# Performance work log

Measured on AMD Instinct MI355X. Metric: run time of the kernel, lower is better.

## Reference

```python
import jax, jax.numpy as jnp
import numpy as np

N = 100000   # nodes
E = 1600000  # edges
NF, EF = 128, 16      # node_features, edge_features
NFIL, EFIL = 64, 32   # node_filters, edge_filters
C = 16                # classes


def setup_inputs() -> dict:
    key = jax.random.key(0)
    ks = jax.random.split(key, 12)
    s = 0.1
    return {
        "x": jax.random.normal(ks[0], (N, NF), jnp.float32),
        "edge_index": jax.random.randint(ks[1], (2, E), 0, N),
        "edge_x": jax.random.normal(ks[2], (E, EF), jnp.float32),
        # edge MLP params
        "W1": jax.random.normal(ks[3], (EF, EFIL), jnp.float32) * s,
        "b1": jnp.zeros((EFIL,), jnp.float32),
        "W2": jax.random.normal(ks[4], (EFIL, 1), jnp.float32) * s,
        "b2": jnp.zeros((1,), jnp.float32),
        # GCN layer params
        "Wc1": jax.random.normal(ks[5], (NF, NFIL), jnp.float32) * s,
        "bc1": jnp.zeros((NFIL,), jnp.float32),
        "Wc2": jax.random.normal(ks[6], (NFIL, C), jnp.float32) * s,
        "bc2": jnp.zeros((C,), jnp.float32),
    }


def gcn_conv(x, src, tgt, w, W, b, n):
    # PyG GCNConv with edge_weight: x @ W, symmetric norm, scatter-add, + bias.
    x = x @ W                                             # [n, out]
    deg = jax.ops.segment_sum(w, tgt, num_segments=n)     # weighted degree incl. self-loops
    dinv = jnp.where(deg > 0, jax.lax.rsqrt(deg), 0.0)
    norm = dinv[src] * w * dinv[tgt]                      # [E+n]
    out = jax.ops.segment_sum(norm[:, None] * x[src], tgt, num_segments=n)
    return out + b


def reference(x, edge_index, edge_x, W1, b1, W2, b2, Wc1, bc1, Wc2, bc2):
    # edge MLP -> scalar attention weight per edge
    h = jax.nn.relu(edge_x @ W1 + b1)
    ew = jax.nn.sigmoid(h @ W2 + b2).reshape(-1)          # [E]
    src, tgt = edge_index[0], edge_index[1]
    # add self-loops with weight 1 (as GCNConv does internally)
    loop = jnp.arange(N)
    src_f = jnp.concatenate([src, loop])
    tgt_f = jnp.concatenate([tgt, loop])
    ew_f = jnp.concatenate([ew, jnp.ones((N,), ew.dtype)])
    h1 = jax.nn.relu(gcn_conv(x, src_f, tgt_f, ew_f, Wc1, bc1, N))
    # dropout omitted: eval mode (F.dropout is identity when training=False)
    h2 = gcn_conv(h1, src_f, tgt_f, ew_f, Wc2, bc2, N)
    return jax.nn.log_softmax(h2, axis=1)
```

## Files before the change

### kernel.cpp

```cpp
#include <hip/hip_runtime.h>
#include <math.h>

#define NFD 128
#define EF_ 16
#define EFIL 32
#define NFIL 64
#define CLS 16

typedef unsigned int uint;
typedef unsigned long long ull;
typedef unsigned short ushort;

__device__ inline void fma4(float4& a, float s, const float4& w) {
  a.x = fmaf(s, w.x, a.x); a.y = fmaf(s, w.y, a.y);
  a.z = fmaf(s, w.z, a.z); a.w = fmaf(s, w.w, a.w);
}

__device__ inline uint bf16_rn(float f) {
  uint u = __float_as_uint(f);
  return (u + 0x7FFFu + ((u >> 16) & 1u)) >> 16;
}
__device__ inline float entw(uint lo) {
  return __uint_as_float((lo >> 17) << 16);
}

__global__ void init_head_kernel(int* __restrict__ head, int n) {
  int i = blockIdx.x * blockDim.x + threadIdx.x;
  if (i < n) head[i] = -1;
}

__global__ __launch_bounds__(256) void edge_mlp_link_kernel(
    const float* __restrict__ edge_x, const int* __restrict__ ei,
    const float* __restrict__ W1, const float* __restrict__ b1,
    const float* __restrict__ W2, const float* __restrict__ b2,
    int* __restrict__ head, ull* __restrict__ nextbuf, int E) {
  __shared__ __align__(16) float sW1[EF_ * EFIL];
  __shared__ float sb1[EFIL];
  __shared__ float sW2[EFIL];
  __shared__ float sb2v;
  int t = threadIdx.x;
  for (int idx = t; idx < EF_ * EFIL / 4; idx += 256)
    reinterpret_cast<float4*>(sW1)[idx] = reinterpret_cast<const float4*>(W1)[idx];
  if (t < EFIL) { sb1[t] = b1[t]; sW2[t] = W2[t]; }
  if (t == 64) sb2v = b2[0];
  __syncthreads();
  int e = blockIdx.x * 256 + t;
  if (e >= E) return;
  const float4* ex4 = reinterpret_cast<const float4*>(edge_x) + (size_t)e * (EF_ / 4);
  float ex[EF_];
  #pragma unroll
  for (int q = 0; q < EF_ / 4; q++) {
    float4 v = ex4[q];
    ex[4*q+0] = v.x; ex[4*q+1] = v.y; ex[4*q+2] = v.z; ex[4*q+3] = v.w;
  }
  float acc[EFIL];
  #pragma unroll
  for (int j = 0; j < EFIL; j++) acc[j] = sb1[j];
  #pragma unroll
  for (int k = 0; k < EF_; k++) {
    float xk = ex[k];
    #pragma unroll
    for (int j4 = 0; j4 < EFIL / 4; j4++) {
      float4 w = reinterpret_cast<const float4*>(sW1)[k * (EFIL/4) + j4];
      acc[4*j4+0] = fmaf(xk, w.x, acc[4*j4+0]);
      acc[4*j4+1] = fmaf(xk, w.y, acc[4*j4+1]);
      acc[4*j4+2] = fmaf(xk, w.z, acc[4*j4+2]);
      acc[4*j4+3] = fmaf(xk, w.w, acc[4*j4+3]);
    }
  }
  float s = sb2v;
  #pragma unroll
  for (int j = 0; j < EFIL; j++) s = fmaf(fmaxf(acc[j], 0.f), sW2[j], s);
  float sig = 1.0f / (1.0f + __expf(-s));
  int sv = ei[e], tg = ei[(size_t)E + e];
  uint lo = ((bf16_rn(sig) & 0x7FFFu) << 17) | (uint)sv;
  int old = atomicExch(&head[tg], e);
  nextbuf[e] = ((ull)(uint)old << 32) | lo;
}

__global__ __launch_bounds__(256) void walk_kernel(
    const int* __restrict__ head, const ull* __restrict__ nextbuf,
    uint* __restrict__ slot, int* __restrict__ grp_cnt,
    float* __restrict__ dinv, int cap, int n) {
  int i = blockIdx.x * blockDim.x + threadIdx.x;
  if (i >= n) return;
  int e = head[i];
  int cnt = 0;
  float sum = 0.f;
  uint* sl = slot + (size_t)i * cap;
  while (e >= 0 && cnt < cap) {
    uint b0 = 0, b1 = 0, b2 = 0, b3 = 0, b4 = 0, b5 = 0, b6 = 0, b7 = 0;
    int k = 0;
    ull v;
    v = nextbuf[e]; b0 = (uint)v; sum += entw(b0); e = (int)(uint)(v >> 32); k = 1;
    if (e >= 0) { v = nextbuf[e]; b1 = (uint)v; sum += entw(b1); e = (int)(uint)(v >> 32); k = 2;
    if (e >= 0) { v = nextbuf[e]; b2 = (uint)v; sum += entw(b2); e = (int)(uint)(v >> 32); k = 3;
    if (e >= 0) { v = nextbuf[e]; b3 = (uint)v; sum += entw(b3); e = (int)(uint)(v >> 32); k = 4;
    if (e >= 0) { v = nextbuf[e]; b4 = (uint)v; sum += entw(b4); e = (int)(uint)(v >> 32); k = 5;
    if (e >= 0) { v = nextbuf[e]; b5 = (uint)v; sum += entw(b5); e = (int)(uint)(v >> 32); k = 6;
    if (e >= 0) { v = nextbuf[e]; b6 = (uint)v; sum += entw(b6); e = (int)(uint)(v >> 32); k = 7;
    if (e >= 0) { v = nextbuf[e]; b7 = (uint)v; sum += entw(b7); e = (int)(uint)(v >> 32); k = 8;
    }}}}}}}
    uint4 lov = {b0, b1, b2, b3};
    uint4 hiv = {b4, b5, b6, b7};
    *reinterpret_cast<uint4*>(sl + cnt) = lov;
    *reinterpret_cast<uint4*>(sl + cnt + 4) = hiv;
    cnt += k;
  }
  grp_cnt[i] = cnt;
  dinv[i] = rsqrtf(1.0f + sum);
}

__global__ __launch_bounds__(256) void gemm1_kernel(
    const float* __restrict__ x, const float* __restrict__ Wc1,
    uint* __restrict__ xwb, int n) {
  __shared__ __align__(16) float sW[NFD * NFIL];
  int t = threadIdx.x;
  for (int idx = t; idx < NFD * NFIL / 4; idx += 256)
    reinterpret_cast<float4*>(sW)[idx] = reinterpret_cast<const float4*>(Wc1)[idx];
  __syncthreads();
  int tc = t & 15;
  int tr = t >> 4;
  int nrb = (n + 31) >> 5;
  const float4* sW4 = reinterpret_cast<const float4*>(sW);
  for (int rb = blockIdx.x; rb < nrb; rb += gridDim.x) {
    int r0 = rb * 32 + tr * 2;
    int r1 = r0 + 1;
    int c0 = r0 < n ? r0 : n - 1;
    int c1 = r1 < n ? r1 : n - 1;
    const float4* xr0 = reinterpret_cast<const float4*>(x + (size_t)c0 * NFD);
    const float4* xr1 = reinterpret_cast<const float4*>(x + (size_t)c1 * NFD);
    float4 a0 = {0, 0, 0, 0}, a1 = {0, 0, 0, 0};
    #pragma unroll 4
    for (int k4 = 0; k4 < NFD / 4; k4++) {
      float4 xa = xr0[k4];
      float4 xb = xr1[k4];
      float4 w0 = sW4[(k4*4+0)*16 + tc];
      float4 w1 = sW4[(k4*4+1)*16 + tc];
      float4 w2 = sW4[(k4*4+2)*16 + tc];
      float4 w3 = sW4[(k4*4+3)*16 + tc];
      fma4(a0, xa.x, w0); fma4(a0, xa.y, w1); fma4(a0, xa.z, w2); fma4(a0, xa.w, w3);
      fma4(a1, xb.x, w0); fma4(a1, xb.y, w1); fma4(a1, xb.z, w2); fma4(a1, xb.w, w3);
    }
    if (r0 < n) {
      uint2 o = {bf16_rn(a0.x) | (bf16_rn(a0.y) << 16),
                 bf16_rn(a0.z) | (bf16_rn(a0.w) << 16)};
      reinterpret_cast<uint2*>(xwb + (size_t)r0 * 32)[tc] = o;
    }
    if (r1 < n) {
      uint2 o = {bf16_rn(a1.x) | (bf16_rn(a1.y) << 16),
                 bf16_rn(a1.z) | (bf16_rn(a1.w) << 16)};
      reinterpret_cast<uint2*>(xwb + (size_t)r1 * 32)[tc] = o;
    }
  }
}

__global__ __launch_bounds__(256) void agg1_fused_kernel(
    const int* __restrict__ grp_cnt, const uint* __restrict__ slot, int cap,
    const float* __restrict__ dinv, const uint* __restrict__ xwb,
    const float* __restrict__ bc1, const float* __restrict__ Wc2,
    ushort* __restrict__ ywb, int n) {
  __shared__ float sh[16][NFIL + 4];
  __shared__ float sW2[NFIL * CLS];
  __shared__ float sb1[NFIL];
  int t = threadIdx.x;
  for (int i = t; i < NFIL * CLS; i += 256) sW2[i] = Wc2[i];
  if (t < NFIL) sb1[t] = bc1[t];
  __syncthreads();
  int r = t >> 4;
  int node = blockIdx.x * 16 + r;
  int f4 = t & 15;
  bool ok = node < n;
  int nd = ok ? node : 0;
  int cnt = ok ? grp_cnt[nd] : 0;
  const uint* base = slot + (size_t)nd * cap;
  const uint2* xw2 = reinterpret_cast<const uint2*>(xwb);
  float d = ok ? dinv[nd] : 0.f;
  uint2 g = xw2[(size_t)nd * 16 + f4];
  float4 acc = {d * __uint_as_float(g.x << 16),
                d * __uint_as_float(g.x & 0xFFFF0000u),
                d * __uint_as_float(g.y << 16),
                d * __uint_as_float(g.y & 0xFFFF0000u)};
  int p = 0;
  for (; p + 1 < cnt; p += 2) {
    uint v0 = base[p], v1 = base[p + 1];
    int s0 = v0 & 0x1FFFF, s1 = v1 & 0x1FFFF;
    float w0 = entw(v0) * dinv[s0];
    float w1 = entw(v1) * dinv[s1];
    uint2 g0 = xw2[(size_t)s0 * 16 + f4];
    uint2 g1 = xw2[(size_t)s1 * 16 + f4];
    acc.x = fmaf(w0, __uint_as_float(g0.x << 16), acc.x);
    acc.y = fmaf(w0, __uint_as_float(g0.x & 0xFFFF0000u), acc.y);
    acc.z = fmaf(w0, __uint_as_float(g0.y << 16), acc.z);
    acc.w = fmaf(w0, __uint_as_float(g0.y & 0xFFFF0000u), acc.w);
    acc.x = fmaf(w1, __uint_as_float(g1.x << 16), acc.x);
    acc.y = fmaf(w1, __uint_as_float(g1.x & 0xFFFF0000u), acc.y);
    acc.z = fmaf(w1, __uint_as_float(g1.y << 16), acc.z);
    acc.w = fmaf(w1, __uint_as_float(g1.y & 0xFFFF0000u), acc.w);
  }
  if (p < cnt) {
    uint v0 = base[p];
    int s0 = v0 & 0x1FFFF;
    float w0 = entw(v0) * dinv[s0];
    uint2 g0 = xw2[(size_t)s0 * 16 + f4];
    acc.x = fmaf(w0, __uint_as_float(g0.x << 16), acc.x);
    acc.y = fmaf(w0, __uint_as_float(g0.x & 0xFFFF0000u), acc.y);
    acc.z = fmaf(w0, __uint_as_float(g0.y << 16), acc.z);
    acc.w = fmaf(w0, __uint_as_float(g0.y & 0xFFFF0000u), acc.w);
  }
  sh[r][4*f4 + 0] = fmaxf(fmaf(d, acc.x, sb1[4*f4 + 0]), 0.f);
  sh[r][4*f4 + 1] = fmaxf(fmaf(d, acc.y, sb1[4*f4 + 1]), 0.f);
  sh[r][4*f4 + 2] = fmaxf(fmaf(d, acc.z, sb1[4*f4 + 2]), 0.f);
  sh[r][4*f4 + 3] = fmaxf(fmaf(d, acc.w, sb1[4*f4 + 3]), 0.f);
  __syncthreads();
  {
    int j = t & 15;
    float o = 0.f;
    #pragma unroll
    for (int k = 0; k < NFIL; k++) o = fmaf(sh[r][k], sW2[k * CLS + j], o);
    if (ok) ywb[(size_t)node * CLS + j] = (ushort)bf16_rn(o);
  }
}

__global__ __launch_bounds__(256) void agg2_fused_kernel(
    const int* __restrict__ grp_cnt, const uint* __restrict__ slot, int cap,
    const float* __restrict__ dinv, const ushort* __restrict__ ywb,
    const float* __restrict__ bc2, float* __restrict__ out, int n) {
  __shared__ float sb2[CLS];
  int t = threadIdx.x;
  if (t < CLS) sb2[t] = bc2[t];
  __syncthreads();
  int node = blockIdx.x * 16 + (t >> 4);
  int j = t & 15;
  bool ok = node < n;
  int nd = ok ? node : 0;
  int cnt = ok ? grp_cnt[nd] : 0;
  const uint* base = slot + (size_t)nd * cap;
  float d = ok ? dinv[nd] : 0.f;
  float acc = d * __uint_as_float((uint)ywb[(size_t)nd * CLS + j] << 16);
  int p = 0;
  for (; p + 1 < cnt; p += 2) {
    uint v0 = base[p], v1 = base[p + 1];
    int s0 = v0 & 0x1FFFF, s1 = v1 & 0x1FFFF;
    float w0 = entw(v0) * dinv[s0];
    float w1 = entw(v1) * dinv[s1];
    float y0 = __uint_as_float((uint)ywb[(size_t)s0 * CLS + j] << 16);
    float y1 = __uint_as_float((uint)ywb[(size_t)s1 * CLS + j] << 16);
    acc = fmaf(w0, y0, acc);
    acc = fmaf(w1, y1, acc);
  }
  if (p < cnt) {
    uint v0 = base[p];
    int s0 = v0 & 0x1FFFF;
    float w0 = entw(v0) * dinv[s0];
    acc = fmaf(w0, __uint_as_float((uint)ywb[(size_t)s0 * CLS + j] << 16), acc);
  }
  float v = fmaf(d, acc, sb2[j]);
  float m = v;
  m = fmaxf(m, __shfl_xor(m, 1, 16));
  m = fmaxf(m, __shfl_xor(m, 2, 16));
  m = fmaxf(m, __shfl_xor(m, 4, 16));
  m = fmaxf(m, __shfl_xor(m, 8, 16));
  float ex = __expf(v - m);
  float ssum = ex;
  ssum += __shfl_xor(ssum, 1, 16);
  ssum += __shfl_xor(ssum, 2, 16);
  ssum += __shfl_xor(ssum, 4, 16);
  ssum += __shfl_xor(ssum, 8, 16);
  if (ok) out[(size_t)node * CLS + j] = (v - m) - __logf(ssum);
}

extern "C" void kernel_launch(void* const* d_in, const int* in_sizes, int n_in,
                              void* d_out, int out_size, void* d_ws, size_t ws_size,
                              hipStream_t stream) {
  const float* x      = (const float*)d_in[0];
  const int*   ei     = (const int*)d_in[1];
  const float* edge_x = (const float*)d_in[2];
  const float* W1     = (const float*)d_in[3];
  const float* b1     = (const float*)d_in[4];
  const float* W2     = (const float*)d_in[5];
  const float* b2     = (const float*)d_in[6];
  const float* Wc1    = (const float*)d_in[7];
  const float* bc1    = (const float*)d_in[8];
  const float* Wc2    = (const float*)d_in[9];
  const float* bc2    = (const float*)d_in[10];
  float* outp = (float*)d_out;
  int n = in_sizes[0] / NFD;
  int E = in_sizes[1] / 2;

  int cap = 48;
  while (cap > 24 && 8.0 * E + (double)n * (172.0 + 4.0 * cap) > (double)ws_size)
    cap -= 8;

  char* base = (char*)d_ws;
  int* head = (int*)base;            base += (size_t)n * 4;
  ull* nextbuf = (ull*)base;         base += (size_t)E * 8;
  uint* slot = (uint*)base;          base += (size_t)n * cap * 4;
  int* grp_cnt = (int*)base;         base += (size_t)n * 4;
  float* dinv = (float*)base;        base += (size_t)n * 4;
  uint* xwb = (uint*)base;           base += (size_t)n * 128;
  ushort* ywb = (ushort*)base;

  int nblk16 = (n + 15) / 16;
  int nblk256 = (n + 255) / 256;
  init_head_kernel<<<nblk256, 256, 0, stream>>>(head, n);
  edge_mlp_link_kernel<<<(E + 255) / 256, 256, 0, stream>>>(
      edge_x, ei, W1, b1, W2, b2, head, nextbuf, E);
  walk_kernel<<<nblk256, 256, 0, stream>>>(head, nextbuf, slot, grp_cnt, dinv, cap, n);
  gemm1_kernel<<<1024, 256, 0, stream>>>(x, Wc1, xwb, n);
  agg1_fused_kernel<<<nblk16, 256, 0, stream>>>(grp_cnt, slot, cap, dinv, xwb, bc1, Wc2, ywb, n);
  agg2_fused_kernel<<<nblk16, 256, 0, stream>>>(grp_cnt, slot, cap, dinv, ywb, bc2, outp, n);
}
```

Before: 228.9 us.

## Split per-node list heads four ways and store neighbor slots column-major

Edge linking now spreads each target node's linked-list head over four sub-heads (chosen by block index), padded to 32 bytes per node, to reduce atomic contention and shorten the dependent pointer chase. The walk kernel follows the four chains in parallel, which gives more memory-level parallelism. It writes neighbor entries into a column-major slot array so that consecutive nodes' entries are adjacent for the aggregation kernels. Head init uses a memset instead of a kernel. The trade-offs are a larger head buffer, and the aggregation reads change from per-node contiguous to strided-by-n, which could hurt per-thread locality even though lanes for different nodes now coalesce.

```diff
diff --git a/kernel.cpp b/kernel.cpp
--- a/kernel.cpp
+++ b/kernel.cpp
@@ -22,11 +22,6 @@
 }
 __device__ inline float entw(uint lo) {
   return __uint_as_float((lo >> 17) << 16);
-}
-
-__global__ void init_head_kernel(int* __restrict__ head, int n) {
-  int i = blockIdx.x * blockDim.x + threadIdx.x;
-  if (i < n) head[i] = -1;
 }
 
 __global__ __launch_bounds__(256) void edge_mlp_link_kernel(
@@ -74,40 +69,40 @@
   float sig = 1.0f / (1.0f + __expf(-s));
   int sv = ei[e], tg = ei[(size_t)E + e];
   uint lo = ((bf16_rn(sig) & 0x7FFFu) << 17) | (uint)sv;
-  int old = atomicExch(&head[tg], e);
+  int old = atomicExch(&head[(size_t)tg * 8 + (blockIdx.x & 3)], e);
   nextbuf[e] = ((ull)(uint)old << 32) | lo;
 }
 
 __global__ __launch_bounds__(256) void walk_kernel(
     const int* __restrict__ head, const ull* __restrict__ nextbuf,
-    uint* __restrict__ slot, int* __restrict__ grp_cnt,
-    float* __restrict__ dinv, int cap, int n) {
+    uint* __restrict__ slotc, int* __restrict__ grp_cnt,
+    float* __restrict__ dinv, int caprows, int n) {
   int i = blockIdx.x * blockDim.x + threadIdx.x;
   if (i >= n) return;
-  int e = head[i];
+  int4 h = *reinterpret_cast<const int4*>(head + (size_t)i * 8);
+  int e0 = h.x, e1 = h.y, e2 = h.z, e3 = h.w;
   int cnt = 0;
   float sum = 0.f;
-  uint* sl = slot + (size_t)i * cap;
-  while (e >= 0 && cnt < cap) {
-    uint b0 = 0, b1 = 0, b2 = 0, b3 = 0, b4 = 0, b5 = 0, b6 = 0, b7 = 0;
-    int k = 0;
-    ull v;
-    v = nextbuf[e]; b0 = (uint)v; sum += entw(b0); e = (int)(uint)(v >> 32); k = 1;
-    if (e >= 0) { v = nextbuf[e]; b1 = (uint)v; sum += entw(b1); e = (int)(uint)(v >> 32); k = 2;
-    if (e >= 0) { v = nextbuf[e]; b2 = (uint)v; sum += entw(b2); e = (int)(uint)(v >> 32); k = 3;
-    if (e >= 0) { v = nextbuf[e]; b3 = (uint)v; sum += entw(b3); e = (int)(uint)(v >> 32); k = 4;
-    if (e >= 0) { v = nextbuf[e]; b4 = (uint)v; sum += entw(b4); e = (int)(uint)(v >> 32); k = 5;
-    if (e >= 0) { v = nextbuf[e]; b5 = (uint)v; sum += entw(b5); e = (int)(uint)(v >> 32); k = 6;
-    if (e >= 0) { v = nextbuf[e]; b6 = (uint)v; sum += entw(b6); e = (int)(uint)(v >> 32); k = 7;
-    if (e >= 0) { v = nextbuf[e]; b7 = (uint)v; sum += entw(b7); e = (int)(uint)(v >> 32); k = 8;
-    }}}}}}}
-    uint4 lov = {b0, b1, b2, b3};
-    uint4 hiv = {b4, b5, b6, b7};
-    *reinterpret_cast<uint4*>(sl + cnt) = lov;
-    *reinterpret_cast<uint4*>(sl + cnt + 4) = hiv;
-    cnt += k;
-  }
-  grp_cnt[i] = cnt;
+  while (e0 >= 0 || e1 >= 0 || e2 >= 0 || e3 >= 0) {
+    ull v0 = 0, v1 = 0, v2 = 0, v3 = 0;
+    if (e0 >= 0) v0 = nextbuf[e0];
+    if (e1 >= 0) v1 = nextbuf[e1];
+    if (e2 >= 0) v2 = nextbuf[e2];
+    if (e3 >= 0) v3 = nextbuf[e3];
+    if (e0 >= 0) { uint lo = (uint)v0; sum += entw(lo);
+      if (cnt < caprows) slotc[(size_t)cnt * n + i] = lo;
+      cnt++; e0 = (int)(uint)(v0 >> 32); }
+    if (e1 >= 0) { uint lo = (uint)v1; sum += entw(lo);
+      if (cnt < caprows) slotc[(size_t)cnt * n + i] = lo;
+      cnt++; e1 = (int)(uint)(v1 >> 32); }
+    if (e2 >= 0) { uint lo = (uint)v2; sum += entw(lo);
+      if (cnt < caprows) slotc[(size_t)cnt * n + i] = lo;
+      cnt++; e2 = (int)(uint)(v2 >> 32); }
+    if (e3 >= 0) { uint lo = (uint)v3; sum += entw(lo);
+      if (cnt < caprows) slotc[(size_t)cnt * n + i] = lo;
+      cnt++; e3 = (int)(uint)(v3 >> 32); }
+  }
+  grp_cnt[i] = min(cnt, caprows);
   dinv[i] = rsqrtf(1.0f + sum);
 }
 
@@ -156,7 +151,7 @@
 }
 
 __global__ __launch_bounds__(256) void agg1_fused_kernel(
-    const int* __restrict__ grp_cnt, const uint* __restrict__ slot, int cap,
+    const int* __restrict__ grp_cnt, const uint* __restrict__ slotc,
     const float* __restrict__ dinv, const uint* __restrict__ xwb,
     const float* __restrict__ bc1, const float* __restrict__ Wc2,
     ushort* __restrict__ ywb, int n) {
@@ -173,7 +168,6 @@
   bool ok = node < n;
   int nd = ok ? node : 0;
   int cnt = ok ? grp_cnt[nd] : 0;
-  const uint* base = slot + (size_t)nd * cap;
   const uint2* xw2 = reinterpret_cast<const uint2*>(xwb);
   float d = ok ? dinv[nd] : 0.f;
   uint2 g = xw2[(size_t)nd * 16 + f4];
@@ -183,7 +177,8 @@
                 d * __uint_as_float(g.y & 0xFFFF0000u)};
   int p = 0;
   for (; p + 1 < cnt; p += 2) {
-    uint v0 = base[p], v1 = base[p + 1];
+    uint v0 = slotc[(size_t)p * n + nd];
+    uint v1 = slotc[(size_t)(p + 1) * n + nd];
     int s0 = v0 & 0x1FFFF, s1 = v1 & 0x1FFFF;
     float w0 = entw(v0) * dinv[s0];
     float w1 = entw(v1) * dinv[s1];
@@ -199,7 +194,7 @@
     acc.w = fmaf(w1, __uint_as_float(g1.y & 0xFFFF0000u), acc.w);
   }
   if (p < cnt) {
-    uint v0 = base[p];
+    uint v0 = slotc[(size_t)p * n + nd];
     int s0 = v0 & 0x1FFFF;
     float w0 = entw(v0) * dinv[s0];
     uint2 g0 = xw2[(size_t)s0 * 16 + f4];
@@ -223,7 +218,7 @@
 }
 
 __global__ __launch_bounds__(256) void agg2_fused_kernel(
-    const int* __restrict__ grp_cnt, const uint* __restrict__ slot, int cap,
+    const int* __restrict__ grp_cnt, const uint* __restrict__ slotc,
     const float* __restrict__ dinv, const ushort* __restrict__ ywb,
     const float* __restrict__ bc2, float* __restrict__ out, int n) {
   __shared__ float sb2[CLS];
@@ -235,12 +230,12 @@
   bool ok = node < n;
   int nd = ok ? node : 0;
   int cnt = ok ? grp_cnt[nd] : 0;
-  const uint* base = slot + (size_t)nd * cap;
   float d = ok ? dinv[nd] : 0.f;
   float acc = d * __uint_as_float((uint)ywb[(size_t)nd * CLS + j] << 16);
   int p = 0;
   for (; p + 1 < cnt; p += 2) {
-    uint v0 = base[p], v1 = base[p + 1];
+    uint v0 = slotc[(size_t)p * n + nd];
+    uint v1 = slotc[(size_t)(p + 1) * n + nd];
     int s0 = v0 & 0x1FFFF, s1 = v1 & 0x1FFFF;
     float w0 = entw(v0) * dinv[s0];
     float w1 = entw(v1) * dinv[s1];
@@ -250,7 +245,7 @@
     acc = fmaf(w1, y1, acc);
   }
   if (p < cnt) {
-    uint v0 = base[p];
+    uint v0 = slotc[(size_t)p * n + nd];
     int s0 = v0 & 0x1FFFF;
     float w0 = entw(v0) * dinv[s0];
     acc = fmaf(w0, __uint_as_float((uint)ywb[(size_t)s0 * CLS + j] << 16), acc);
@@ -289,13 +284,13 @@
   int E = in_sizes[1] / 2;
 
   int cap = 48;
-  while (cap > 24 && 8.0 * E + (double)n * (172.0 + 4.0 * cap) > (double)ws_size)
+  while (cap > 32 && 8.0 * E + (double)n * (200.0 + 4.0 * cap) > (double)ws_size)
     cap -= 8;
 
   char* base = (char*)d_ws;
-  int* head = (int*)base;            base += (size_t)n * 4;
+  int* head = (int*)base;            base += (size_t)n * 32;
   ull* nextbuf = (ull*)base;         base += (size_t)E * 8;
-  uint* slot = (uint*)base;          base += (size_t)n * cap * 4;
+  uint* slotc = (uint*)base;         base += (size_t)n * cap * 4;
   int* grp_cnt = (int*)base;         base += (size_t)n * 4;
   float* dinv = (float*)base;        base += (size_t)n * 4;
   uint* xwb = (uint*)base;           base += (size_t)n * 128;
@@ -303,11 +298,11 @@
 
   int nblk16 = (n + 15) / 16;
   int nblk256 = (n + 255) / 256;
-  init_head_kernel<<<nblk256, 256, 0, stream>>>(head, n);
+  hipMemsetAsync(head, 0xFF, (size_t)n * 32, stream);
   edge_mlp_link_kernel<<<(E + 255) / 256, 256, 0, stream>>>(
       edge_x, ei, W1, b1, W2, b2, head, nextbuf, E);
-  walk_kernel<<<nblk256, 256, 0, stream>>>(head, nextbuf, slot, grp_cnt, dinv, cap, n);
+  walk_kernel<<<nblk256, 256, 0, stream>>>(head, nextbuf, slotc, grp_cnt, dinv, cap, n);
   gemm1_kernel<<<1024, 256, 0, stream>>>(x, Wc1, xwb, n);
-  agg1_fused_kernel<<<nblk16, 256, 0, stream>>>(grp_cnt, slot, cap, dinv, xwb, bc1, Wc2, ywb, n);
-  agg2_fused_kernel<<<nblk16, 256, 0, stream>>>(grp_cnt, slot, cap, dinv, ywb, bc2, outp, n);
-}
+  agg1_fused_kernel<<<nblk16, 256, 0, stream>>>(grp_cnt, slotc, dinv, xwb, bc1, Wc2, ywb, n);
+  agg2_fused_kernel<<<nblk16, 256, 0, stream>>>(grp_cnt, slotc, dinv, ywb, bc2, outp, n);
+}
```

Measured after the change: 231.6 us. About the same (+1.2%).
